# Kernel tuning notes

Hardware: AMD Instinct MI355X
Metric: run time of the kernel (lower is better)

Reference implementation:

```python
import jax, jax.numpy as jnp
import numpy as np
from jax import lax

K = 9          # box kernel side
PAD = K // 2   # same padding
K_SUM = float(K * K * K)


def _box_sum(x):
    """Sliding-window sum over a 9x9x9 box, zero-padded (separable 1D convs).
    x: [B, 1, D, H, W] -> same shape."""
    dn = ('NCDHW', 'OIDHW', 'NCDHW')
    for ax in range(3):  # D, H, W
        kshape = [1, 1, 1, 1, 1]
        kshape[2 + ax] = K
        w = jnp.ones(kshape, dtype=x.dtype)
        pad = [(0, 0), (0, 0), (0, 0)]
        pad[ax] = (PAD, PAD)
        x = lax.conv_general_dilated(x, w, window_strides=(1, 1, 1),
                                     padding=pad, dimension_numbers=dn)
    return x


def setup_inputs() -> dict:
    key = jax.random.key(0)
    k1, k2 = jax.random.split(key)
    shape = (2, 1, 192, 192, 192)  # [B, 1, D, H, W]
    I = jax.random.uniform(k1, shape, dtype=jnp.float32)
    J = jax.random.uniform(k2, shape, dtype=jnp.float32)
    return {"I": I, "J": J}


def reference(I, J):
    II = I * I
    JJ = J * J
    IJ = I * J
    I_sum = _box_sum(I)
    J_sum = _box_sum(J)
    II_sum = _box_sum(II)
    JJ_sum = _box_sum(JJ)
    IJ_sum = _box_sum(IJ)
    I_u = I / K_SUM
    J_u = J / K_SUM
    cross = IJ_sum - I_sum * J_u - J_sum * I_u + I_u * J_u * K_SUM
    I_var = II_sum - 2 * I_sum * I_u + I_u * I_u * K_SUM
    J_var = JJ_sum - 2 * J_sum * J_u + J_u * J_u * K_SUM
    top = cross * cross
    bottom = I_var * J_var + 1e-5
    return -jnp.mean(top / bottom)
```

## Files before the change

### kernel.cpp

```cpp
#include <hip/hip_runtime.h>
#include <hip/hip_bf16.h>

#define WDIM 192
#define PLANE (192 * 192)
#define VOL (192 * 192 * 192)
#define HC 16
#define TR (HC + 8)
#define NCH 12
#define RWU 100
#define DC 24

typedef __fp16 h2f __attribute__((ext_vector_type(2)));

__global__ void zero_out_k(float* out) { out[0] = 0.0f; }

static __device__ inline unsigned int pk_h16(float a, float b) {
    h2f v = __builtin_amdgcn_cvt_pkrtz(a, b);
    return __builtin_bit_cast(unsigned int, v);
}
static __device__ inline float dot2u(unsigned int a, unsigned int b, float c) {
    return __builtin_amdgcn_fdot2(__builtin_bit_cast(h2f, a),
                                  __builtin_bit_cast(h2f, b), c, false);
}

static __device__ inline unsigned int pk_bf16(float a, float b) {
    union { __hip_bfloat162 v; unsigned int u; } cvt;
    cvt.v = __float22bfloat162_rn(make_float2(a, b));
    return cvt.u;
}
static __device__ inline float bf_lo(unsigned int u) {
    union { unsigned int u; float f; } c; c.u = u << 16; return c.f;
}
static __device__ inline float bf_hi(unsigned int u) {
    union { unsigned int u; float f; } c; c.u = u & 0xffff0000u; return c.f;
}

__global__ __launch_bounds__(192) void wh_pass(const float* __restrict__ I,
                                               const float* __restrict__ J,
                                               unsigned int* __restrict__ B) {
    __shared__ unsigned int sI[TR * RWU];
    __shared__ unsigned int sJ[TR * RWU];
    const int t = threadIdx.x;
    const int d = blockIdx.x / NCH;
    const int c = blockIdx.x - d * NCH;
    const int h0 = c * HC;

    const size_t bofs = (size_t)blockIdx.y * VOL;
    const float* Ib = I + bofs;
    const float* Jb = J + bofs;
    unsigned int* Bb = B + bofs * 3;

    const size_t dbase = (size_t)d * PLANE;

    {
        const int row = t >> 3;
        const int p = t & 7;
        unsigned int* dst = (p < 4) ? sI : sJ;
        const int q = p & 3;
        const int col = (q < 2) ? q : (96 + q);
        dst[row * RWU + col] = 0u;
    }

    #pragma unroll
    for (int i = 0; i < 6; ++i) {
        const int idx4 = i * 192 + t;
        const int row  = idx4 / 48;
        const int col4 = (idx4 - row * 48) * 4;
        const int h = h0 - 4 + row;
        float4 vI = make_float4(0.f, 0.f, 0.f, 0.f);
        float4 vJ = vI;
        if (h >= 0 && h < WDIM) {
            vI = *(const float4*)(Ib + dbase + (size_t)h * WDIM + col4);
            vJ = *(const float4*)(Jb + dbase + (size_t)h * WDIM + col4);
        }
        uint2 uI, uJ;
        uI.x = pk_h16(vI.x, vI.y); uI.y = pk_h16(vI.z, vI.w);
        uJ.x = pk_h16(vJ.x, vJ.y); uJ.y = pk_h16(vJ.z, vJ.w);
        const int ui = row * RWU + 2 + (col4 >> 1);
        *(uint2*)&sI[ui] = uI;
        *(uint2*)&sJ[ui] = uJ;
    }
    __syncthreads();

    const int tb = t >> 1;
    const int odd = t & 1;
    const unsigned int ONESF = 0x3C003C00u;
    const unsigned int ones0 = odd ? 0x3C000000u : ONESF;
    const unsigned int ones4 = odd ? ONESF : 0x00003C00u;
    const unsigned int keep0 = odd ? 0xFFFF0000u : 0xFFFFFFFFu;
    const unsigned int keep4 = odd ? 0xFFFFFFFFu : 0x0000FFFFu;

    float ring0[9], ring1[9], ring2[9], ring3[9], ring4[9];
    #pragma unroll
    for (int j = 0; j < 9; ++j) { ring0[j]=0.f; ring1[j]=0.f; ring2[j]=0.f; ring3[j]=0.f; ring4[j]=0.f; }
    float s0 = 0.f, s1 = 0.f, s2 = 0.f, s3 = 0.f, s4 = 0.f;

    unsigned int AI[5], AJ[5], BI[5], BJ[5];
    #pragma unroll
    for (int p = 0; p < 5; ++p) { AI[p] = sI[tb + p]; AJ[p] = sJ[tb + p]; }

    #pragma unroll
    for (int s = 0; s < TR; ++s) {
        if (s + 1 < TR) {
            const int base = (s + 1) * RWU + tb;
            if ((s & 1) == 0) {
                #pragma unroll
                for (int p = 0; p < 5; ++p) { BI[p] = sI[base + p]; BJ[p] = sJ[base + p]; }
            } else {
                #pragma unroll
                for (int p = 0; p < 5; ++p) { AI[p] = sI[base + p]; AJ[p] = sJ[base + p]; }
            }
        }
        const unsigned int c0 = ((s & 1) == 0) ? AI[0] : BI[0];
        const unsigned int c1 = ((s & 1) == 0) ? AI[1] : BI[1];
        const unsigned int c2 = ((s & 1) == 0) ? AI[2] : BI[2];
        const unsigned int c3 = ((s & 1) == 0) ? AI[3] : BI[3];
        const unsigned int c4 = ((s & 1) == 0) ? AI[4] : BI[4];
        const unsigned int e0 = ((s & 1) == 0) ? AJ[0] : BJ[0];
        const unsigned int e1 = ((s & 1) == 0) ? AJ[1] : BJ[1];
        const unsigned int e2 = ((s & 1) == 0) ? AJ[2] : BJ[2];
        const unsigned int e3 = ((s & 1) == 0) ? AJ[3] : BJ[3];
        const unsigned int e4 = ((s & 1) == 0) ? AJ[4] : BJ[4];

        const unsigned int mI0 = c0 & keep0, mI4 = c4 & keep4;
        const unsigned int mJ0 = e0 & keep0, mJ4 = e4 & keep4;

        float w0 = dot2u(c0, ones0, 0.f);
        w0 = dot2u(c1, ONESF, w0); w0 = dot2u(c2, ONESF, w0);
        w0 = dot2u(c3, ONESF, w0); w0 = dot2u(c4, ones4, w0);

        float w1 = dot2u(e0, ones0, 0.f);
        w1 = dot2u(e1, ONESF, w1); w1 = dot2u(e2, ONESF, w1);
        w1 = dot2u(e3, ONESF, w1); w1 = dot2u(e4, ones4, w1);

        float w2 = dot2u(mI0, c0, 0.f);
        w2 = dot2u(c1, c1, w2); w2 = dot2u(c2, c2, w2);
        w2 = dot2u(c3, c3, w2); w2 = dot2u(mI4, c4, w2);

        float w3 = dot2u(mJ0, e0, 0.f);
        w3 = dot2u(e1, e1, w3); w3 = dot2u(e2, e2, w3);
        w3 = dot2u(e3, e3, w3); w3 = dot2u(mJ4, e4, w3);

        float w4 = dot2u(mI0, e0, 0.f);
        w4 = dot2u(c1, e1, w4); w4 = dot2u(c2, e2, w4);
        w4 = dot2u(c3, e3, w4); w4 = dot2u(mI4, e4, w4);

        const int j = s % 9;
        s0 += w0 - ring0[j]; ring0[j] = w0;
        s1 += w1 - ring1[j]; ring1[j] = w1;
        s2 += w2 - ring2[j]; ring2[j] = w2;
        s3 += w3 - ring3[j]; ring3[j] = w3;
        s4 += w4 - ring4[j]; ring4[j] = w4;

        if (s >= 8) {
            const int h_out = h0 + s - 8;
            const size_t idx = dbase + (size_t)h_out * WDIM + t;
            uint3 q;
            q.x = pk_bf16(s0, s1);
            q.y = pk_bf16(s2, s3);
            q.z = pk_bf16(s4, 0.f);
            *(uint3*)(Bb + idx * 3) = q;
        }
    }
}

__global__ __launch_bounds__(192) void d_pass(const unsigned int* __restrict__ B,
                                              const float* __restrict__ I,
                                              const float* __restrict__ J,
                                              float* __restrict__ out) {
    const int t = threadIdx.x;
    const int h = blockIdx.x >> 3;
    const int c = blockIdx.x & 7;
    const int d0 = c * DC;
    const int base_h = h * WDIM + t;

    const size_t bofs = (size_t)blockIdx.y * VOL;
    const float* Ib = I + bofs;
    const float* Jb = J + bofs;
    const unsigned int* Bb = B + bofs * 3;

    float r0[9], r1[9], r2[9], r3[9], r4[9];
    #pragma unroll
    for (int j = 0; j < 9; ++j) { r0[j]=0.f; r1[j]=0.f; r2[j]=0.f; r3[j]=0.f; r4[j]=0.f; }
    float s0 = 0.f, s1 = 0.f, s2 = 0.f, s3 = 0.f, s4 = 0.f;

    const float inv_k = 1.0f / 729.0f;
    float local = 0.f;

    uint3 qA[8], qB[8];
    float2 cA[8], cB[8];
    #pragma unroll
    for (int i = 0; i < 8; ++i) {
        const int d_in = d0 - 4 + i;
        qA[i] = make_uint3(0u, 0u, 0u);
        if (d_in >= 0 && d_in < WDIM)
            qA[i] = *(const uint3*)(Bb + ((size_t)d_in * PLANE + base_h) * 3);
        cA[i] = make_float2(0.f, 0.f);
    }

    #pragma unroll
    for (int g = 0; g < 4; ++g) {
        if (g + 1 < 4) {
            #pragma unroll
            for (int i = 0; i < 8; ++i) {
                const int s = (g + 1) * 8 + i;
                const int d_in = d0 - 4 + s;
                uint3 v = make_uint3(0u, 0u, 0u);
                if (d_in >= 0 && d_in < WDIM)
                    v = *(const uint3*)(Bb + ((size_t)d_in * PLANE + base_h) * 3);
                const int d_out = d0 + s - 8;
                const size_t cidx = (size_t)d_out * PLANE + base_h;
                const float ci = Ib[cidx];
                const float cj = Jb[cidx];
                if ((g & 1) == 0) { qB[i] = v; cB[i] = make_float2(ci, cj); }
                else              { qA[i] = v; cA[i] = make_float2(ci, cj); }
            }
        }
        #pragma unroll
        for (int i = 0; i < 8; ++i) {
            const int s = g * 8 + i;
            const uint3 q = ((g & 1) == 0) ? qA[i] : qB[i];
            const float f0 = bf_lo(q.x), f1 = bf_hi(q.x);
            const float f2 = bf_lo(q.y), f3 = bf_hi(q.y);
            const float f4 = bf_lo(q.z);
            const int j = s % 9;
            s0 += f0 - r0[j]; r0[j] = f0;
            s1 += f1 - r1[j]; r1[j] = f1;
            s2 += f2 - r2[j]; r2[j] = f2;
            s3 += f3 - r3[j]; r3[j] = f3;
            s4 += f4 - r4[j]; r4[j] = f4;

            if (s >= 8) {
                const float2 cc = ((g & 1) == 0) ? cA[i] : cB[i];
                const float Iu = cc.x * inv_k;
                const float Ju = cc.y * inv_k;
                const float cross = s4 - s0 * Ju - s1 * Iu + Iu * Ju * 729.0f;
                const float Ivar  = s2 - 2.0f * s0 * Iu + Iu * Iu * 729.0f;
                const float Jvar  = s3 - 2.0f * s1 * Ju + Ju * Ju * 729.0f;
                local += (cross * cross) / (Ivar * Jvar + 1e-5f);
            }
        }
    }

    __shared__ float sred[192];
    sred[t] = local;
    __syncthreads();
    if (t < 64) {
        float v = sred[t] + sred[t + 64] + sred[t + 128];
        #pragma unroll
        for (int off = 32; off; off >>= 1) v += __shfl_down(v, off);
        if (t == 0) {
            atomicAdd(out, v * (-1.0f / 14155776.0f));
        }
    }
}

extern "C" void kernel_launch(void* const* d_in, const int* in_sizes, int n_in,
                              void* d_out, int out_size, void* d_ws, size_t ws_size,
                              hipStream_t stream) {
    const float* I = (const float*)d_in[0];
    const float* J = (const float*)d_in[1];
    float* out = (float*)d_out;
    unsigned int* B = (unsigned int*)d_ws;

    zero_out_k<<<1, 1, 0, stream>>>(out);

    const size_t need2 = (size_t)2 * VOL * 12;
    if (ws_size >= need2) {
        wh_pass<<<dim3(192 * NCH, 2), 192, 0, stream>>>(I, J, B);
        d_pass <<<dim3(1536, 2), 192, 0, stream>>>(B, I, J, out);
    } else {
        for (int b = 0; b < 2; ++b) {
            const float* Ib = I + (size_t)b * VOL;
            const float* Jb = J + (size_t)b * VOL;
            wh_pass<<<dim3(192 * NCH, 1), 192, 0, stream>>>(Ib, Jb, B);
            d_pass <<<dim3(1536, 1), 192, 0, stream>>>(B, Ib, Jb, out);
        }
    }
}
```

Before: 233.5 us.

## Double H-chunk height, interleave I/J in shared memory, fold output zeroing into wh_pass

Each wh_pass block now covers 32 H rows instead of 16, which halves the number of blocks and lowers the share of the 8-row halo that has to be reloaded. The I and J fp16 pairs now sit interleaved in a single uint2 shared array, so one 64-bit LDS read returns both operands and the staging writes become 128-bit. The separate zero_out kernel launch is gone; thread 0 of block 0 in wh_pass zeroes the output instead. In exchange, each block uses more shared memory and has a longer serial row loop, and the grid is smaller, which may lower occupancy or parallelism.

```diff
diff --git a/kernel.cpp b/kernel.cpp
--- a/kernel.cpp
+++ b/kernel.cpp
@@ -4,15 +4,13 @@
 #define WDIM 192
 #define PLANE (192 * 192)
 #define VOL (192 * 192 * 192)
-#define HC 16
+#define HC 32
 #define TR (HC + 8)
-#define NCH 12
-#define RWU 100
+#define NCH 6
+#define RW2 100
 #define DC 24
 
 typedef __fp16 h2f __attribute__((ext_vector_type(2)));
-
-__global__ void zero_out_k(float* out) { out[0] = 0.0f; }
 
 static __device__ inline unsigned int pk_h16(float a, float b) {
     h2f v = __builtin_amdgcn_cvt_pkrtz(a, b);
@@ -37,14 +35,16 @@
 
 __global__ __launch_bounds__(192) void wh_pass(const float* __restrict__ I,
                                                const float* __restrict__ J,
-                                               unsigned int* __restrict__ B) {
-    __shared__ unsigned int sI[TR * RWU];
-    __shared__ unsigned int sJ[TR * RWU];
+                                               unsigned int* __restrict__ B,
+                                               float* __restrict__ out0) {
+    __shared__ uint2 sIJ[TR * RW2];
     const int t = threadIdx.x;
     const int d = blockIdx.x / NCH;
     const int c = blockIdx.x - d * NCH;
     const int h0 = c * HC;
 
+    if (out0 && blockIdx.x == 0 && blockIdx.y == 0 && t == 0) *out0 = 0.0f;
+
     const size_t bofs = (size_t)blockIdx.y * VOL;
     const float* Ib = I + bofs;
     const float* Jb = J + bofs;
@@ -52,17 +52,15 @@
 
     const size_t dbase = (size_t)d * PLANE;
 
-    {
-        const int row = t >> 3;
-        const int p = t & 7;
-        unsigned int* dst = (p < 4) ? sI : sJ;
-        const int q = p & 3;
+    if (t < TR * 4) {
+        const int row = t >> 2;
+        const int q = t & 3;
         const int col = (q < 2) ? q : (96 + q);
-        dst[row * RWU + col] = 0u;
-    }
-
-    #pragma unroll
-    for (int i = 0; i < 6; ++i) {
+        sIJ[row * RW2 + col] = make_uint2(0u, 0u);
+    }
+
+    #pragma unroll
+    for (int i = 0; i < TR * 48 / 192; ++i) {
         const int idx4 = i * 192 + t;
         const int row  = idx4 / 48;
         const int col4 = (idx4 - row * 48) * 4;
@@ -73,12 +71,13 @@
             vI = *(const float4*)(Ib + dbase + (size_t)h * WDIM + col4);
             vJ = *(const float4*)(Jb + dbase + (size_t)h * WDIM + col4);
         }
-        uint2 uI, uJ;
-        uI.x = pk_h16(vI.x, vI.y); uI.y = pk_h16(vI.z, vI.w);
-        uJ.x = pk_h16(vJ.x, vJ.y); uJ.y = pk_h16(vJ.z, vJ.w);
-        const int ui = row * RWU + 2 + (col4 >> 1);
-        *(uint2*)&sI[ui] = uI;
-        *(uint2*)&sJ[ui] = uJ;
+        uint4 u;
+        u.x = pk_h16(vI.x, vI.y);
+        u.y = pk_h16(vJ.x, vJ.y);
+        u.z = pk_h16(vI.z, vI.w);
+        u.w = pk_h16(vJ.z, vJ.w);
+        const int e = row * RW2 + 2 + (col4 >> 1);
+        *(uint4*)&sIJ[e] = u;
     }
     __syncthreads();
 
@@ -95,32 +94,29 @@
     for (int j = 0; j < 9; ++j) { ring0[j]=0.f; ring1[j]=0.f; ring2[j]=0.f; ring3[j]=0.f; ring4[j]=0.f; }
     float s0 = 0.f, s1 = 0.f, s2 = 0.f, s3 = 0.f, s4 = 0.f;
 
-    unsigned int AI[5], AJ[5], BI[5], BJ[5];
-    #pragma unroll
-    for (int p = 0; p < 5; ++p) { AI[p] = sI[tb + p]; AJ[p] = sJ[tb + p]; }
+    uint2 PA[5], PB[5];
+    #pragma unroll
+    for (int p = 0; p < 5; ++p) PA[p] = sIJ[tb + p];
 
     #pragma unroll
     for (int s = 0; s < TR; ++s) {
         if (s + 1 < TR) {
-            const int base = (s + 1) * RWU + tb;
+            const int base = (s + 1) * RW2 + tb;
             if ((s & 1) == 0) {
                 #pragma unroll
-                for (int p = 0; p < 5; ++p) { BI[p] = sI[base + p]; BJ[p] = sJ[base + p]; }
+                for (int p = 0; p < 5; ++p) PB[p] = sIJ[base + p];
             } else {
                 #pragma unroll
-                for (int p = 0; p < 5; ++p) { AI[p] = sI[base + p]; AJ[p] = sJ[base + p]; }
+                for (int p = 0; p < 5; ++p) PA[p] = sIJ[base + p];
             }
         }
-        const unsigned int c0 = ((s & 1) == 0) ? AI[0] : BI[0];
-        const unsigned int c1 = ((s & 1) == 0) ? AI[1] : BI[1];
-        const unsigned int c2 = ((s & 1) == 0) ? AI[2] : BI[2];
-        const unsigned int c3 = ((s & 1) == 0) ? AI[3] : BI[3];
-        const unsigned int c4 = ((s & 1) == 0) ? AI[4] : BI[4];
-        const unsigned int e0 = ((s & 1) == 0) ? AJ[0] : BJ[0];
-        const unsigned int e1 = ((s & 1) == 0) ? AJ[1] : BJ[1];
-        const unsigned int e2 = ((s & 1) == 0) ? AJ[2] : BJ[2];
-        const unsigned int e3 = ((s & 1) == 0) ? AJ[3] : BJ[3];
-        const unsigned int e4 = ((s & 1) == 0) ? AJ[4] : BJ[4];
+        const uint2 g0 = ((s & 1) == 0) ? PA[0] : PB[0];
+        const uint2 g1 = ((s & 1) == 0) ? PA[1] : PB[1];
+        const uint2 g2 = ((s & 1) == 0) ? PA[2] : PB[2];
+        const uint2 g3 = ((s & 1) == 0) ? PA[3] : PB[3];
+        const uint2 g4 = ((s & 1) == 0) ? PA[4] : PB[4];
+        const unsigned int c0 = g0.x, c1 = g1.x, c2 = g2.x, c3 = g3.x, c4 = g4.x;
+        const unsigned int e0 = g0.y, e1 = g1.y, e2 = g2.y, e3 = g3.y, e4 = g4.y;
 
         const unsigned int mI0 = c0 & keep0, mI4 = c4 & keep4;
         const unsigned int mJ0 = e0 & keep0, mJ4 = e4 & keep4;
@@ -263,17 +259,16 @@
     float* out = (float*)d_out;
     unsigned int* B = (unsigned int*)d_ws;
 
-    zero_out_k<<<1, 1, 0, stream>>>(out);
-
     const size_t need2 = (size_t)2 * VOL * 12;
     if (ws_size >= need2) {
-        wh_pass<<<dim3(192 * NCH, 2), 192, 0, stream>>>(I, J, B);
+        wh_pass<<<dim3(WDIM * NCH, 2), 192, 0, stream>>>(I, J, B, out);
         d_pass <<<dim3(1536, 2), 192, 0, stream>>>(B, I, J, out);
     } else {
         for (int b = 0; b < 2; ++b) {
             const float* Ib = I + (size_t)b * VOL;
             const float* Jb = J + (size_t)b * VOL;
-            wh_pass<<<dim3(192 * NCH, 1), 192, 0, stream>>>(Ib, Jb, B);
+            wh_pass<<<dim3(WDIM * NCH, 1), 192, 0, stream>>>(Ib, Jb, B,
+                                                             b == 0 ? out : nullptr);
             d_pass <<<dim3(1536, 1), 192, 0, stream>>>(B, Ib, Jb, out);
         }
     }
```

Result: no change. 234.4 us (+0.4%).
